# Kernel tuning notes

Measured on AMD Instinct MI355X. Metric: run time of the kernel, lower is better.

## Reference

```python
import jax, jax.numpy as jnp
import numpy as np

# Module config (from init_kwargs): causal=False, window_size=(256,256), window_type=0,
# softmax_scale=None -> 1/sqrt(D), dropout=0 (eval mode).
WINDOW_LEFT, WINDOW_RIGHT = 256, 256


def _window_mask(Sq, Sk, causal, use_window_mask):
    """Boolean [Sq, Sk] visibility mask, FA2 semantics (right-aligned offset)."""
    qi = jnp.arange(Sq)[:, None]
    kj = jnp.arange(Sk)[None, :]
    offset = Sk - Sq
    if causal:
        return kj <= qi + offset  # window (-1, 0)
    if use_window_mask:
        m = jnp.ones((Sq, Sk), dtype=bool)
        if WINDOW_LEFT >= 0:
            m = m & (kj >= qi + offset - WINDOW_LEFT)
        if WINDOW_RIGHT >= 0:
            m = m & (kj <= qi + offset + WINDOW_RIGHT)
        return m
    return None  # full attention


def setup_inputs() -> dict:
    key = jax.random.key(0)
    kq, kkv = jax.random.split(key)
    B, Sq, Sk, H, D = 2, 2048, 2048, 16, 64
    q = jax.random.normal(kq, (B, Sq, H, D), dtype=jnp.float32)
    kv = jax.random.normal(kkv, (B, Sk, 2, H, D), dtype=jnp.float32)
    return {"q": q, "kv": kv, "causal": 0, "use_window_mask": 1, "return_attn_probs": 0}


def reference(q, kv, causal, use_window_mask, return_attn_probs):
    # q: (B, Sq, H, D); kv: (B, Sk, 2, H, D)
    B, Sq, H, D = q.shape
    Sk = kv.shape[1]
    k = kv[:, :, 0]  # (B, Sk, H, D)
    v = kv[:, :, 1]
    scale = 1.0 / (D ** 0.5)
    scores = jnp.einsum('bqhd,bkhd->bhqk', q, k) * scale  # (B, H, Sq, Sk)
    mask = _window_mask(Sq, Sk, bool(causal), bool(use_window_mask))
    if mask is not None:
        scores = jnp.where(mask[None, None], scores, jnp.finfo(scores.dtype).min)
    probs = jax.nn.softmax(scores, axis=-1)
    out = jnp.einsum('bhqk,bkhd->bqhd', probs, v)  # (B, Sq, H, D)
    return out
```

## Files before the change

### kernel.cpp

```cpp
#include <hip/hip_runtime.h>
#include <hip/hip_bf16.h>

#define B_    2
#define SQ_   2048
#define SK_   2048
#define NH_   16
#define DH_   64
#define WIN_  256
#define NEG_  -30000.0f

typedef __bf16 bf16_t;
typedef bf16_t bf16x8 __attribute__((ext_vector_type(8)));
typedef bf16_t bf16x4 __attribute__((ext_vector_type(4)));
typedef float  f32x4  __attribute__((ext_vector_type(4)));

#define KSTRIDE 72
#define VSTRIDE 72
#define PSTRIDE 72

__global__ __launch_bounds__(256, 2)
void fa_fwd(const float* __restrict__ qg, const float* __restrict__ kvg,
            float* __restrict__ outg) {
  const int tid  = threadIdx.x;
  const int wid  = tid >> 6;
  const int lane = tid & 63;
  const int quad = lane >> 4;
  const int li   = lane & 15;

  const int bid = blockIdx.x;
  const int qb  = bid >> 5;
  const int bh  = bid & 31;
  const int b   = bh >> 4;
  const int h   = bh & 15;

  const int q0b = qb * 128;
  const int q0  = q0b + wid * 32;

  __shared__ __align__(16) bf16_t sK [64 * KSTRIDE];
  __shared__ __align__(16) bf16_t sVT[64 * VSTRIDE];
  __shared__ __align__(16) bf16_t sP [4 * 32 * PSTRIDE];
  bf16_t* pl = sP + wid * 32 * PSTRIDE;

  const float qscale = 0.125f * 1.44269504088896340736f;
  bf16x8 qfrag[2][2];
#pragma unroll
  for (int qt = 0; qt < 2; ++qt) {
    const float* qrow = qg + ((size_t)((b * SQ_ + q0 + qt * 16 + li) * NH_ + h)) * DH_;
#pragma unroll
    for (int c = 0; c < 2; ++c) {
      f32x4 a0 = *(const f32x4*)(qrow + c * 32 + quad * 8);
      f32x4 a1 = *(const f32x4*)(qrow + c * 32 + quad * 8 + 4);
#pragma unroll
      for (int i = 0; i < 4; ++i) {
        qfrag[qt][c][i]     = (bf16_t)(a0[i] * qscale);
        qfrag[qt][c][i + 4] = (bf16_t)(a1[i] * qscale);
      }
    }
  }

  f32x4 oacc[2][4];
#pragma unroll
  for (int qt = 0; qt < 2; ++qt)
#pragma unroll
    for (int t = 0; t < 4; ++t) { f32x4 z = {0.f, 0.f, 0.f, 0.f}; oacc[qt][t] = z; }
  float m[2] = {NEG_, NEG_}, l[2] = {0.f, 0.f};

  int klo = q0b - WIN_; if (klo < 0) klo = 0;
  int khi = q0b + 127 + WIN_ + 1; if (khi > SK_) khi = SK_;

  const float* kbase = kvg + (size_t)b * SK_ * 2 * NH_ * DH_ + (size_t)h * DH_;
  const float* vbase = kbase + NH_ * DH_;
  const size_t krow_stride = 2 * NH_ * DH_;

  const int skey = tid >> 2;
  const int sd0  = (tid & 3) * 16;

  f32x4 ka[4], va[4];
  {
    const float* kr = kbase + (size_t)(klo + skey) * krow_stride + sd0;
    const float* vr = vbase + (size_t)(klo + skey) * krow_stride + sd0;
#pragma unroll
    for (int i = 0; i < 4; ++i) { ka[i] = *(const f32x4*)(kr + 4 * i); va[i] = *(const f32x4*)(vr + 4 * i); }
  }

  for (int kk = klo; kk < khi; kk += 64) {
    {
      bf16x8 w0, w1;
#pragma unroll
      for (int i = 0; i < 4; ++i) {
        w0[i] = (bf16_t)ka[0][i]; w0[i + 4] = (bf16_t)ka[1][i];
        w1[i] = (bf16_t)ka[2][i]; w1[i + 4] = (bf16_t)ka[3][i];
      }
      *(bf16x8*)(sK + skey * KSTRIDE + sd0)     = w0;
      *(bf16x8*)(sK + skey * KSTRIDE + sd0 + 8) = w1;
#pragma unroll
      for (int i = 0; i < 4; ++i)
#pragma unroll
        for (int j = 0; j < 4; ++j)
          sVT[(sd0 + 4 * i + j) * VSTRIDE + skey] = (bf16_t)va[i][j];
    }
    __syncthreads();

    if (kk + 64 < khi) {
      const float* kr = kbase + (size_t)(kk + 64 + skey) * krow_stride + sd0;
      const float* vr = vbase + (size_t)(kk + 64 + skey) * krow_stride + sd0;
#pragma unroll
      for (int i = 0; i < 4; ++i) { ka[i] = *(const f32x4*)(kr + 4 * i); va[i] = *(const f32x4*)(vr + 4 * i); }
    }

    f32x4 sc[2][4];
#pragma unroll
    for (int s = 0; s < 4; ++s) {
      bf16x8 kf0 = *(const bf16x8*)(sK + (s * 16 + li) * KSTRIDE + quad * 8);
      bf16x8 kf1 = *(const bf16x8*)(sK + (s * 16 + li) * KSTRIDE + 32 + quad * 8);
#pragma unroll
      for (int qt = 0; qt < 2; ++qt) {
        f32x4 acc = {0.f, 0.f, 0.f, 0.f};
        acc = __builtin_amdgcn_mfma_f32_16x16x32_bf16(kf0, qfrag[qt][0], acc, 0, 0, 0);
        acc = __builtin_amdgcn_mfma_f32_16x16x32_bf16(kf1, qfrag[qt][1], acc, 0, 0, 0);
        sc[qt][s] = acc;
      }
    }

    float alpha[2];
#pragma unroll
    for (int qt = 0; qt < 2; ++qt) {
      const int qa = q0 + qt * 16 + li;
#pragma unroll
      for (int s = 0; s < 4; ++s)
#pragma unroll
        for (int r = 0; r < 4; ++r) {
          int key = kk + s * 16 + quad * 4 + r;
          unsigned dd = (unsigned)(key - qa + WIN_);
          if (dd > 2u * WIN_) sc[qt][s][r] = NEG_;
        }
      float tmax = NEG_;
#pragma unroll
      for (int s = 0; s < 4; ++s)
        tmax = fmaxf(tmax, fmaxf(fmaxf(sc[qt][s][0], sc[qt][s][1]),
                                 fmaxf(sc[qt][s][2], sc[qt][s][3])));
      tmax = fmaxf(tmax, __shfl_xor(tmax, 16));
      tmax = fmaxf(tmax, __shfl_xor(tmax, 32));
      float mnew = fmaxf(m[qt], tmax);
      alpha[qt] = exp2f(m[qt] - mnew);
      float psum = 0.f;
#pragma unroll
      for (int s = 0; s < 4; ++s) {
        bf16x4 pk;
#pragma unroll
        for (int r = 0; r < 4; ++r) {
          float p = exp2f(sc[qt][s][r] - mnew);
          psum += p;
          pk[r] = (bf16_t)p;
        }
        *(bf16x4*)(pl + (qt * 16 + li) * PSTRIDE + s * 16 + quad * 4) = pk;
      }
      psum += __shfl_xor(psum, 16);
      psum += __shfl_xor(psum, 32);
      l[qt] = l[qt] * alpha[qt] + psum;
      m[qt] = mnew;
    }

    asm volatile("s_waitcnt lgkmcnt(0)" ::: "memory");

#pragma unroll
    for (int qt = 0; qt < 2; ++qt) {
      float al[4];
#pragma unroll
      for (int r = 0; r < 4; ++r) al[r] = __shfl(alpha[qt], quad * 4 + r);
#pragma unroll
      for (int t = 0; t < 4; ++t) {
        oacc[qt][t][0] *= al[0]; oacc[qt][t][1] *= al[1];
        oacc[qt][t][2] *= al[2]; oacc[qt][t][3] *= al[3];
      }
    }

#pragma unroll
    for (int kc = 0; kc < 2; ++kc) {
      bf16x8 pf0 = *(const bf16x8*)(pl + li * PSTRIDE + kc * 32 + quad * 8);
      bf16x8 pf1 = *(const bf16x8*)(pl + (16 + li) * PSTRIDE + kc * 32 + quad * 8);
#pragma unroll
      for (int t = 0; t < 4; ++t) {
        bf16x8 vf = *(const bf16x8*)(sVT + (16 * t + li) * VSTRIDE + kc * 32 + quad * 8);
        oacc[0][t] = __builtin_amdgcn_mfma_f32_16x16x32_bf16(pf0, vf, oacc[0][t], 0, 0, 0);
        oacc[1][t] = __builtin_amdgcn_mfma_f32_16x16x32_bf16(pf1, vf, oacc[1][t], 0, 0, 0);
      }
    }
    __syncthreads();
  }

#pragma unroll
  for (int qt = 0; qt < 2; ++qt) {
    float rl[4];
#pragma unroll
    for (int r = 0; r < 4; ++r) {
      float lv = __shfl(l[qt], quad * 4 + r);
      rl[r] = 1.0f / lv;
    }
    float* orow = outg + ((size_t)((b * SQ_ + q0 + qt * 16) * NH_ + h)) * DH_;
#pragma unroll
    for (int t = 0; t < 4; ++t)
#pragma unroll
      for (int r = 0; r < 4; ++r)
        orow[(size_t)(quad * 4 + r) * (NH_ * DH_) + 16 * t + li] = oacc[qt][t][r] * rl[r];
  }
}

extern "C" void kernel_launch(void* const* d_in, const int* in_sizes, int n_in,
                              void* d_out, int out_size, void* d_ws, size_t ws_size,
                              hipStream_t stream) {
  (void)in_sizes; (void)n_in; (void)out_size; (void)d_ws; (void)ws_size;
  const float* q  = (const float*)d_in[0];
  const float* kv = (const float*)d_in[1];
  float* out = (float*)d_out;
  dim3 grid(B_ * NH_ * (SQ_ / 128));
  fa_fwd<<<grid, 256, 0, stream>>>(q, kv, out);
}
```

Baseline: 119.3 us.

## Double-buffer K/V tiles, keep P in registers, skip out-of-window tiles per wave

Double-buffers the K and transposed-V shared tiles so one barrier per iteration suffices and the next tile's global loads overlap compute. V is now loaded coalesced along D and transposed via an XOR-swizzled layout. The P round-trip through shared memory is removed by packing probabilities directly into MFMA operand registers with a matching V fragment permutation. Each wave skips key tiles entirely outside its window and skips masking for fully-inside tiles; it also uses native exp2 and raises occupancy to 3 blocks. This increases index complexity and register pressure.

```diff
diff --git a/kernel.cpp b/kernel.cpp
--- a/kernel.cpp
+++ b/kernel.cpp
@@ -16,9 +16,8 @@
 
 #define KSTRIDE 72
 #define VSTRIDE 72
-#define PSTRIDE 72
-
-__global__ __launch_bounds__(256, 2)
+
+__global__ __launch_bounds__(256, 3)
 void fa_fwd(const float* __restrict__ qg, const float* __restrict__ kvg,
             float* __restrict__ outg) {
   const int tid  = threadIdx.x;
@@ -36,10 +35,8 @@
   const int q0b = qb * 128;
   const int q0  = q0b + wid * 32;
 
-  __shared__ __align__(16) bf16_t sK [64 * KSTRIDE];
-  __shared__ __align__(16) bf16_t sVT[64 * VSTRIDE];
-  __shared__ __align__(16) bf16_t sP [4 * 32 * PSTRIDE];
-  bf16_t* pl = sP + wid * 32 * PSTRIDE;
+  __shared__ __align__(16) bf16_t sK [2][64 * KSTRIDE];
+  __shared__ __align__(16) bf16_t sVT[2][64 * VSTRIDE];
 
   const float qscale = 0.125f * 1.44269504088896340736f;
   bf16x8 qfrag[2][2];
@@ -70,123 +67,131 @@
 
   const float* kbase = kvg + (size_t)b * SK_ * 2 * NH_ * DH_ + (size_t)h * DH_;
   const float* vbase = kbase + NH_ * DH_;
-  const size_t krow_stride = 2 * NH_ * DH_;
+  const size_t krow = 2 * NH_ * DH_;
 
   const int skey = tid >> 2;
   const int sd0  = (tid & 3) * 16;
-
-  f32x4 ka[4], va[4];
-  {
-    const float* kr = kbase + (size_t)(klo + skey) * krow_stride + sd0;
-    const float* vr = vbase + (size_t)(klo + skey) * krow_stride + sd0;
-#pragma unroll
-    for (int i = 0; i < 4; ++i) { ka[i] = *(const f32x4*)(kr + 4 * i); va[i] = *(const f32x4*)(vr + 4 * i); }
-  }
+  const int vg   = (lane >> 3) & 7;
+
+  bf16x8 kpre[2], vpre[2];
+
+  auto load_tile = [&](int kt) {
+    const float* kr = kbase + (size_t)(kt + skey) * krow + sd0;
+    f32x4 a0 = *(const f32x4*)kr,      a1 = *(const f32x4*)(kr + 4);
+    f32x4 a2 = *(const f32x4*)(kr + 8), a3 = *(const f32x4*)(kr + 12);
+#pragma unroll
+    for (int i = 0; i < 4; ++i) {
+      kpre[0][i] = (bf16_t)a0[i]; kpre[0][i + 4] = (bf16_t)a1[i];
+      kpre[1][i] = (bf16_t)a2[i]; kpre[1][i + 4] = (bf16_t)a3[i];
+    }
+    const float* vr = vbase + (size_t)(kt + wid * 16) * krow + lane;
+#pragma unroll
+    for (int o = 0; o < 2; ++o)
+#pragma unroll
+      for (int j = 0; j < 8; ++j)
+        vpre[o][j] = (bf16_t)vr[(size_t)(o * 8 + j) * krow];
+  };
+  auto stage = [&](bf16_t* sKb, bf16_t* sVb) {
+    *(bf16x8*)&sKb[skey * KSTRIDE + sd0]     = kpre[0];
+    *(bf16x8*)&sKb[skey * KSTRIDE + sd0 + 8] = kpre[1];
+#pragma unroll
+    for (int o = 0; o < 2; ++o)
+      *(bf16x8*)&sVb[lane * VSTRIDE + (((2 * wid + o) ^ vg) << 3)] = vpre[o];
+  };
+
+  bf16_t *sKc = sK[0], *sVc = sVT[0], *sKn = sK[1], *sVn = sVT[1];
+
+  load_tile(klo);
+  stage(sKc, sVc);
+  __syncthreads();
 
   for (int kk = klo; kk < khi; kk += 64) {
-    {
-      bf16x8 w0, w1;
-#pragma unroll
-      for (int i = 0; i < 4; ++i) {
-        w0[i] = (bf16_t)ka[0][i]; w0[i + 4] = (bf16_t)ka[1][i];
-        w1[i] = (bf16_t)ka[2][i]; w1[i + 4] = (bf16_t)ka[3][i];
-      }
-      *(bf16x8*)(sK + skey * KSTRIDE + sd0)     = w0;
-      *(bf16x8*)(sK + skey * KSTRIDE + sd0 + 8) = w1;
-#pragma unroll
-      for (int i = 0; i < 4; ++i)
-#pragma unroll
-        for (int j = 0; j < 4; ++j)
-          sVT[(sd0 + 4 * i + j) * VSTRIDE + skey] = (bf16_t)va[i][j];
-    }
+    const bool nxt = (kk + 64 < khi);
+    if (nxt) load_tile(kk + 64);
+
+    if (kk + 63 >= q0 - WIN_ && kk <= q0 + 31 + WIN_) {
+      f32x4 sc[2][4];
+#pragma unroll
+      for (int s = 0; s < 4; ++s) {
+        const int row = (s * 16 + li) * KSTRIDE;
+        bf16x8 kf0 = *(const bf16x8*)&sKc[row + quad * 8];
+        bf16x8 kf1 = *(const bf16x8*)&sKc[row + 32 + quad * 8];
+#pragma unroll
+        for (int qt = 0; qt < 2; ++qt) {
+          f32x4 acc = {0.f, 0.f, 0.f, 0.f};
+          acc = __builtin_amdgcn_mfma_f32_16x16x32_bf16(kf0, qfrag[qt][0], acc, 0, 0, 0);
+          acc = __builtin_amdgcn_mfma_f32_16x16x32_bf16(kf1, qfrag[qt][1], acc, 0, 0, 0);
+          sc[qt][s] = acc;
+        }
+      }
+      float alpha[2];
+      bf16x8 pa[2][2];
+#pragma unroll
+      for (int qt = 0; qt < 2; ++qt) {
+        const int t0 = q0 + qt * 16;
+        if (kk < t0 - 241 || kk > t0 + 193) {
+          const int qa = t0 + li;
+#pragma unroll
+          for (int s = 0; s < 4; ++s)
+#pragma unroll
+            for (int r = 0; r < 4; ++r) {
+              int key = kk + s * 16 + quad * 4 + r;
+              unsigned dd = (unsigned)(key - qa + WIN_);
+              if (dd > 2u * WIN_) sc[qt][s][r] = NEG_;
+            }
+        }
+        float tmax = NEG_;
+#pragma unroll
+        for (int s = 0; s < 4; ++s)
+          tmax = fmaxf(tmax, fmaxf(fmaxf(sc[qt][s][0], sc[qt][s][1]),
+                                   fmaxf(sc[qt][s][2], sc[qt][s][3])));
+        tmax = fmaxf(tmax, __shfl_xor(tmax, 16));
+        tmax = fmaxf(tmax, __shfl_xor(tmax, 32));
+        float mnew = fmaxf(m[qt], tmax);
+        alpha[qt] = __builtin_amdgcn_exp2f(m[qt] - mnew);
+        float psum = 0.f;
+#pragma unroll
+        for (int s = 0; s < 4; ++s)
+#pragma unroll
+          for (int r = 0; r < 4; ++r) {
+            float p = __builtin_amdgcn_exp2f(sc[qt][s][r] - mnew);
+            psum += p;
+            pa[qt][s >> 1][(s & 1) * 4 + r] = (bf16_t)p;
+          }
+        psum += __shfl_xor(psum, 16);
+        psum += __shfl_xor(psum, 32);
+        l[qt] = l[qt] * alpha[qt] + psum;
+        m[qt] = mnew;
+        float al[4];
+#pragma unroll
+        for (int r = 0; r < 4; ++r) al[r] = __shfl(alpha[qt], quad * 4 + r);
+#pragma unroll
+        for (int t = 0; t < 4; ++t) {
+          oacc[qt][t][0] *= al[0]; oacc[qt][t][1] *= al[1];
+          oacc[qt][t][2] *= al[2]; oacc[qt][t][3] *= al[3];
+        }
+      }
+#pragma unroll
+      for (int kc = 0; kc < 2; ++kc) {
+        const int olo = kc * 4 + (quad >> 1);
+#pragma unroll
+        for (int t = 0; t < 4; ++t) {
+          const int d = 16 * t + li;
+          const int g = (d >> 3) & 7;
+          const int rowo = d * VSTRIDE + (quad & 1) * 4;
+          bf16x4 lo = *(const bf16x4*)&sVc[rowo + ((olo       ^ g) << 3)];
+          bf16x4 hi = *(const bf16x4*)&sVc[rowo + (((olo + 2) ^ g) << 3)];
+          bf16x8 vf = {lo[0], lo[1], lo[2], lo[3], hi[0], hi[1], hi[2], hi[3]};
+          oacc[0][t] = __builtin_amdgcn_mfma_f32_16x16x32_bf16(pa[0][kc], vf, oacc[0][t], 0, 0, 0);
+          oacc[1][t] = __builtin_amdgcn_mfma_f32_16x16x32_bf16(pa[1][kc], vf, oacc[1][t], 0, 0, 0);
+        }
+      }
+    }
+
+    if (nxt) stage(sKn, sVn);
     __syncthreads();
-
-    if (kk + 64 < khi) {
-      const float* kr = kbase + (size_t)(kk + 64 + skey) * krow_stride + sd0;
-      const float* vr = vbase + (size_t)(kk + 64 + skey) * krow_stride + sd0;
-#pragma unroll
-      for (int i = 0; i < 4; ++i) { ka[i] = *(const f32x4*)(kr + 4 * i); va[i] = *(const f32x4*)(vr + 4 * i); }
-    }
-
-    f32x4 sc[2][4];
-#pragma unroll
-    for (int s = 0; s < 4; ++s) {
-      bf16x8 kf0 = *(const bf16x8*)(sK + (s * 16 + li) * KSTRIDE + quad * 8);
-      bf16x8 kf1 = *(const bf16x8*)(sK + (s * 16 + li) * KSTRIDE + 32 + quad * 8);
-#pragma unroll
-      for (int qt = 0; qt < 2; ++qt) {
-        f32x4 acc = {0.f, 0.f, 0.f, 0.f};
-        acc = __builtin_amdgcn_mfma_f32_16x16x32_bf16(kf0, qfrag[qt][0], acc, 0, 0, 0);
-        acc = __builtin_amdgcn_mfma_f32_16x16x32_bf16(kf1, qfrag[qt][1], acc, 0, 0, 0);
-        sc[qt][s] = acc;
-      }
-    }
-
-    float alpha[2];
-#pragma unroll
-    for (int qt = 0; qt < 2; ++qt) {
-      const int qa = q0 + qt * 16 + li;
-#pragma unroll
-      for (int s = 0; s < 4; ++s)
-#pragma unroll
-        for (int r = 0; r < 4; ++r) {
-          int key = kk + s * 16 + quad * 4 + r;
-          unsigned dd = (unsigned)(key - qa + WIN_);
-          if (dd > 2u * WIN_) sc[qt][s][r] = NEG_;
-        }
-      float tmax = NEG_;
-#pragma unroll
-      for (int s = 0; s < 4; ++s)
-        tmax = fmaxf(tmax, fmaxf(fmaxf(sc[qt][s][0], sc[qt][s][1]),
-                                 fmaxf(sc[qt][s][2], sc[qt][s][3])));
-      tmax = fmaxf(tmax, __shfl_xor(tmax, 16));
-      tmax = fmaxf(tmax, __shfl_xor(tmax, 32));
-      float mnew = fmaxf(m[qt], tmax);
-      alpha[qt] = exp2f(m[qt] - mnew);
-      float psum = 0.f;
-#pragma unroll
-      for (int s = 0; s < 4; ++s) {
-        bf16x4 pk;
-#pragma unroll
-        for (int r = 0; r < 4; ++r) {
-          float p = exp2f(sc[qt][s][r] - mnew);
-          psum += p;
-          pk[r] = (bf16_t)p;
-        }
-        *(bf16x4*)(pl + (qt * 16 + li) * PSTRIDE + s * 16 + quad * 4) = pk;
-      }
-      psum += __shfl_xor(psum, 16);
-      psum += __shfl_xor(psum, 32);
-      l[qt] = l[qt] * alpha[qt] + psum;
-      m[qt] = mnew;
-    }
-
-    asm volatile("s_waitcnt lgkmcnt(0)" ::: "memory");
-
-#pragma unroll
-    for (int qt = 0; qt < 2; ++qt) {
-      float al[4];
-#pragma unroll
-      for (int r = 0; r < 4; ++r) al[r] = __shfl(alpha[qt], quad * 4 + r);
-#pragma unroll
-      for (int t = 0; t < 4; ++t) {
-        oacc[qt][t][0] *= al[0]; oacc[qt][t][1] *= al[1];
-        oacc[qt][t][2] *= al[2]; oacc[qt][t][3] *= al[3];
-      }
-    }
-
-#pragma unroll
-    for (int kc = 0; kc < 2; ++kc) {
-      bf16x8 pf0 = *(const bf16x8*)(pl + li * PSTRIDE + kc * 32 + quad * 8);
-      bf16x8 pf1 = *(const bf16x8*)(pl + (16 + li) * PSTRIDE + kc * 32 + quad * 8);
-#pragma unroll
-      for (int t = 0; t < 4; ++t) {
-        bf16x8 vf = *(const bf16x8*)(sVT + (16 * t + li) * VSTRIDE + kc * 32 + quad * 8);
-        oacc[0][t] = __builtin_amdgcn_mfma_f32_16x16x32_bf16(pf0, vf, oacc[0][t], 0, 0, 0);
-        oacc[1][t] = __builtin_amdgcn_mfma_f32_16x16x32_bf16(pf1, vf, oacc[1][t], 0, 0, 0);
-      }
-    }
-    __syncthreads();
+    bf16_t* t0 = sKc; sKc = sKn; sKn = t0;
+    bf16_t* t1 = sVc; sVc = sVn; sVn = t1;
   }
 
 #pragma unroll
```

Result: faster. 112.1 us (-6.0%).
